# Kernel tuning notes

Hardware: AMD Instinct MI355X
Metric: run time of the kernel (lower is better)

Reference implementation:

```python
import jax, jax.numpy as jnp
import numpy as np

NUM_CEPS = 13  # default num_ceps in log_mel_to_cepstral


def _dct_basis(n_mels, num_ceps):
    # Orthonormal DCT-II basis (scipy.fftpack.dct type=2, norm='ortho'),
    # truncated to the first num_ceps rows. Shape (num_ceps, n_mels).
    n = jnp.arange(n_mels, dtype=jnp.float32)
    k = jnp.arange(num_ceps, dtype=jnp.float32)
    basis = jnp.cos(jnp.pi * (n[None, :] + 0.5) * k[:, None] / n_mels)
    scale = jnp.where(k == 0, jnp.sqrt(1.0 / n_mels), jnp.sqrt(2.0 / n_mels))
    return basis * scale[:, None]


def _log_mel_to_cepstral(mel, basis):
    # mel: (B, 1, F, T) -> cepstral (B, num_ceps, T) with CMVN over (B*T)
    x = jnp.log1p(jnp.abs(mel[:, 0]))                 # (B, F, T)
    c = jnp.einsum('kf,bft->bkt', basis, x)           # (B, num_ceps, T)
    mean = jnp.mean(c, axis=(0, 2), keepdims=True)
    # torch .std is unbiased (ddof=1) over the B*T flattened samples
    std = jnp.std(c, axis=(0, 2), keepdims=True, ddof=1) + 1e-6
    return (c - mean) / std


def setup_inputs() -> dict:
    key = jax.random.key(0)
    k1, k2 = jax.random.split(key)
    B, F, T = 64, 128, 4096
    mel_true = jax.random.normal(k1, (B, 1, F, T), dtype=jnp.float32)
    mel_pred = jax.random.normal(k2, (B, 1, F, T), dtype=jnp.float32)
    return {"mel_true": mel_true, "mel_pred": mel_pred}


def reference(mel_true, mel_pred):
    n_mels = mel_true.shape[2]
    basis = _dct_basis(n_mels, NUM_CEPS)
    c_true = _log_mel_to_cepstral(mel_true, basis)
    c_pred = _log_mel_to_cepstral(mel_pred, basis)
    diff = c_true - c_pred
    mse_dist = jnp.sum(diff * diff, axis=1)           # (B, T)
    log_base_10 = 10.0 / jnp.log(jnp.float32(10.0))
    mcd = log_base_10 * jnp.sqrt(2.0 * mse_dist)
    return jnp.mean(mcd)
```

## Files before the change

### kernel.cpp

```cpp
#include <hip/hip_runtime.h>
#include <math.h>

#define BB 64
#define FF 128
#define TT 4096
#define KK 13
#define NT (BB * TT)
#define NPAIR (NT / 2)
#define MCD_C  6.14185100f



#define KLIST(X) X(0) X(1) X(2) X(3) X(4) X(5) X(6) X(7) X(8) X(9) X(10) X(11) X(12)
#define K12(X)        X(1) X(2) X(3) X(4) X(5) X(6) X(7) X(8) X(9) X(10) X(11) X(12)

__global__ __launch_bounds__(256)
__attribute__((amdgpu_waves_per_eu(4, 4)))
void pass1_kernel(
    const float* __restrict__ melT, const float* __restrict__ melP,
    float* __restrict__ sums, float* __restrict__ cT, float* __restrict__ cP)
{
    const int tensor = blockIdx.x >> 9;
    const int gp = ((blockIdx.x & 511) << 8) + threadIdx.x;
    const float* __restrict__ src = tensor ? melP : melT;
    float* __restrict__ dst = tensor ? cP : cT;

    const int g0 = gp << 1;
    const int b  = g0 >> 12;
    const int t0 = g0 & (TT - 1);
    const float* p = src + (size_t)b * (FF * TT) + t0;

#define DECLACC(i) float ax##i = 0.f, ay##i = 0.f;
    KLIST(DECLACC)
#undef DECLACC

    for (int f0 = 0; f0 < FF; f0 += 8) {
        float2 v[8];
#pragma unroll
        for (int j = 0; j < 8; ++j)
            v[j] = *(const float2*)(p + (size_t)(f0 + j) * TT);

#pragma unroll
        for (int j = 0; j < 8; ++j) {
            const float xx = __log2f(1.0f + fabsf(v[j].x));
            const float xy = __log2f(1.0f + fabsf(v[j].y));

            const float b1 = __cosf((3.14159265358979f / 128.0f) *
                                    ((float)(f0 + j) + 0.5f));
            const float tw = b1 + b1;
            const float b2  = fmaf(tw, b1,  -1.0f);
            const float b3  = fmaf(tw, b2,  -b1);
            const float b4  = fmaf(tw, b3,  -b2);
            const float b5  = fmaf(tw, b4,  -b3);
            const float b6  = fmaf(tw, b5,  -b4);
            const float b7  = fmaf(tw, b6,  -b5);
            const float b8  = fmaf(tw, b7,  -b6);
            const float b9  = fmaf(tw, b8,  -b7);
            const float b10 = fmaf(tw, b9,  -b8);
            const float b11 = fmaf(tw, b10, -b9);
            const float b12 = fmaf(tw, b11, -b10);

            ax0 += xx; ay0 += xy;
#define FMAK(i) ax##i = fmaf(b##i, xx, ax##i); ay##i = fmaf(b##i, xy, ay##i);
            K12(FMAK)
#undef FMAK
        }
    }

#define STK(i) ((float2*)(dst + (size_t)(i) * NT))[gp] = make_float2(ax##i, ay##i);
    KLIST(STK)
#undef STK

    __shared__ float red[4][26];
    const int lane = threadIdx.x & 63;
    const int wave = threadIdx.x >> 6;
#define REDK(i) { \
        float s = ax##i + ay##i; \
        float q = fmaf(ax##i, ax##i, ay##i * ay##i); \
        for (int o = 32; o > 0; o >>= 1) { \
            s += __shfl_down(s, o); q += __shfl_down(q, o); } \
        if (lane == 0) { red[wave][i] = s; red[wave][13 + i] = q; } }
    KLIST(REDK)
#undef REDK
    __syncthreads();
    if (threadIdx.x < 26) {
        const float v = red[0][threadIdx.x] + red[1][threadIdx.x] +
                        red[2][threadIdx.x] + red[3][threadIdx.x];
        atomicAdd(&sums[(tensor * 26 + threadIdx.x) * 16], v);
    }
}

__global__ __launch_bounds__(256, 4) void pass2_kernel(
    const float* __restrict__ sums, const float* __restrict__ cT,
    const float* __restrict__ cP, float* __restrict__ partials)
{
    __shared__ float mT[13], iT[13], mP[13], iP[13];
    if (threadIdx.x < 26) {
        const int tns = threadIdx.x >= 13;
        const int k   = threadIdx.x - tns * 13;
        const float s = sums[(tns * 26 + k) * 16];
        const float q = sums[(tns * 26 + 13 + k) * 16];
        const float N = (float)NT;
        const float m = s / N;
        const float var = fmaxf((q - s * m) / (N - 1.0f), 0.0f);
        const float isd = 1.0f / (sqrtf(var) + 1e-6f);
        if (tns == 0) { mT[k] = m; iT[k] = isd; }
        else          { mP[k] = m; iP[k] = isd; }
    }
    __syncthreads();

    const int gp = blockIdx.x * 256 + threadIdx.x;
    float ssx = 0.0f, ssy = 0.0f;
#pragma unroll
    for (int k = 0; k < KK; ++k) {
        const float2 a = ((const float2*)(cT + (size_t)k * NT))[gp];
        const float2 p = ((const float2*)(cP + (size_t)k * NT))[gp];
        const float dx = (a.x - mT[k]) * iT[k] - (p.x - mP[k]) * iP[k];
        const float dy = (a.y - mT[k]) * iT[k] - (p.y - mP[k]) * iP[k];
        ssx = fmaf(dx, dx, ssx);
        ssy = fmaf(dy, dy, ssy);
    }
    float v = MCD_C * (sqrtf(ssx) + sqrtf(ssy));

    const int lane = threadIdx.x & 63;
    const int wave = threadIdx.x >> 6;
    for (int o = 32; o > 0; o >>= 1) v += __shfl_down(v, o);
    __shared__ float r2[4];
    if (lane == 0) r2[wave] = v;
    __syncthreads();
    if (threadIdx.x == 0)
        partials[blockIdx.x] = r2[0] + r2[1] + r2[2] + r2[3];
}

__global__ __launch_bounds__(256) void pass3_kernel(
    const float* __restrict__ partials, float* __restrict__ out)
{
    float v = partials[threadIdx.x] + partials[threadIdx.x + 256];
    const int lane = threadIdx.x & 63;
    const int wave = threadIdx.x >> 6;
    for (int o = 32; o > 0; o >>= 1) v += __shfl_down(v, o);
    __shared__ float r2[4];
    if (lane == 0) r2[wave] = v;
    __syncthreads();
    if (threadIdx.x == 0)
        out[0] = (r2[0] + r2[1] + r2[2] + r2[3]) * (1.0f / (float)NT);
}

extern "C" void kernel_launch(void* const* d_in, const int* in_sizes, int n_in,
                              void* d_out, int out_size, void* d_ws, size_t ws_size,
                              hipStream_t stream) {
    const float* melT = (const float*)d_in[0];
    const float* melP = (const float*)d_in[1];
    float* out      = (float*)d_out;
    float* sums     = (float*)d_ws;
    float* partials = (float*)((char*)d_ws + 4096);
    float* cT       = (float*)((char*)d_ws + 8192);
    float* cP       = cT + (size_t)KK * NT;

    hipMemsetAsync(d_ws, 0, 4096, stream);

    pass1_kernel<<<1024, 256, 0, stream>>>(melT, melP, sums, cT, cP);
    pass2_kernel<<<512, 256, 0, stream>>>(sums, cT, cP, partials);
    pass3_kernel<<<1, 256, 0, stream>>>(partials, out);
}
```

Before: 287.3 us.

## Fuse MCD passes into one cooperative kernel with grid sync, keeping cepstra in registers

Replaces the three-pass pipeline with a single cooperative kernel. Each thread handles one time column for both tensors, keeps its 13 cepstral coefficients in registers, and after a grid-wide sync applies CMVN and the MCD reduction. This removes the intermediate cepstral writes and re-reads (about 27 MB of traffic) and two kernel launches. The costs are a grid barrier, double the per-thread register state, and a fallback path that recomputes everything if the cooperative launch fails. Reductions now use DPP instead of shuffles.

```diff
diff --git a/kernel.cpp b/kernel.cpp
--- a/kernel.cpp
+++ b/kernel.cpp
@@ -1,149 +1,200 @@
 #include <hip/hip_runtime.h>
+#include <hip/hip_cooperative_groups.h>
 #include <math.h>
+
+namespace cg = cooperative_groups;
 
 #define BB 64
 #define FF 128
 #define TT 4096
 #define KK 13
 #define NT (BB * TT)
-#define NPAIR (NT / 2)
+#define NBLK 1024
 #define MCD_C  6.14185100f
 
 
-
-#define KLIST(X) X(0) X(1) X(2) X(3) X(4) X(5) X(6) X(7) X(8) X(9) X(10) X(11) X(12)
-#define K12(X)        X(1) X(2) X(3) X(4) X(5) X(6) X(7) X(8) X(9) X(10) X(11) X(12)
-
-__global__ __launch_bounds__(256)
-__attribute__((amdgpu_waves_per_eu(4, 4)))
-void pass1_kernel(
-    const float* __restrict__ melT, const float* __restrict__ melP,
-    float* __restrict__ sums, float* __restrict__ cT, float* __restrict__ cP)
-{
-    const int tensor = blockIdx.x >> 9;
-    const int gp = ((blockIdx.x & 511) << 8) + threadIdx.x;
-    const float* __restrict__ src = tensor ? melP : melT;
-    float* __restrict__ dst = tensor ? cP : cT;
-
-    const int g0 = gp << 1;
-    const int b  = g0 >> 12;
-    const int t0 = g0 & (TT - 1);
-    const float* p = src + (size_t)b * (FF * TT) + t0;
-
-#define DECLACC(i) float ax##i = 0.f, ay##i = 0.f;
-    KLIST(DECLACC)
-#undef DECLACC
-
-    for (int f0 = 0; f0 < FF; f0 += 8) {
-        float2 v[8];
-#pragma unroll
-        for (int j = 0; j < 8; ++j)
-            v[j] = *(const float2*)(p + (size_t)(f0 + j) * TT);
-
-#pragma unroll
-        for (int j = 0; j < 8; ++j) {
-            const float xx = __log2f(1.0f + fabsf(v[j].x));
-            const float xy = __log2f(1.0f + fabsf(v[j].y));
-
-            const float b1 = __cosf((3.14159265358979f / 128.0f) *
-                                    ((float)(f0 + j) + 0.5f));
-            const float tw = b1 + b1;
-            const float b2  = fmaf(tw, b1,  -1.0f);
-            const float b3  = fmaf(tw, b2,  -b1);
-            const float b4  = fmaf(tw, b3,  -b2);
-            const float b5  = fmaf(tw, b4,  -b3);
-            const float b6  = fmaf(tw, b5,  -b4);
-            const float b7  = fmaf(tw, b6,  -b5);
-            const float b8  = fmaf(tw, b7,  -b6);
-            const float b9  = fmaf(tw, b8,  -b7);
-            const float b10 = fmaf(tw, b9,  -b8);
-            const float b11 = fmaf(tw, b10, -b9);
-            const float b12 = fmaf(tw, b11, -b10);
-
-            ax0 += xx; ay0 += xy;
-#define FMAK(i) ax##i = fmaf(b##i, xx, ax##i); ay##i = fmaf(b##i, xy, ay##i);
-            K12(FMAK)
-#undef FMAK
+template <int CTRL>
+__device__ __forceinline__ float dpp_add(float x) {
+    return x + __int_as_float(__builtin_amdgcn_update_dpp(
+                   0, __float_as_int(x), CTRL, 0xf, 0xf, true));
+}
+__device__ __forceinline__ float wave_sum(float x) {
+    x = dpp_add<0x111>(x);
+    x = dpp_add<0x112>(x);
+    x = dpp_add<0x114>(x);
+    x = dpp_add<0x118>(x);
+    x = dpp_add<0x142>(x);
+    x = dpp_add<0x143>(x);
+    return x;
+}
+
+__device__ __forceinline__ float agent_load(const float* p) {
+    return __hip_atomic_load(p, __ATOMIC_RELAXED, __HIP_MEMORY_SCOPE_AGENT);
+}
+
+__device__ __forceinline__ void load8(const float* __restrict__ p, int f0,
+                                      float (&v)[8]) {
+#pragma unroll
+    for (int j = 0; j < 8; ++j) v[j] = p[(size_t)(f0 + j) * TT];
+}
+
+__device__ __forceinline__ void comp8(int f0, const float (&vT)[8],
+                                      const float (&vP)[8],
+                                      float (&aT)[KK], float (&aP)[KK]) {
+#pragma unroll
+    for (int j = 0; j < 8; ++j) {
+        const float xT = __log2f(1.0f + fabsf(vT[j]));
+        const float xP = __log2f(1.0f + fabsf(vP[j]));
+        float bk[KK];
+        bk[0] = 1.0f;
+        bk[1] = __cosf((3.14159265358979f / 128.0f) * ((float)(f0 + j) + 0.5f));
+        const float tw = bk[1] + bk[1];
+#pragma unroll
+        for (int k = 2; k < KK; ++k) bk[k] = fmaf(tw, bk[k - 1], -bk[k - 2]);
+#pragma unroll
+        for (int k = 0; k < KK; ++k) {
+            aT[k] = fmaf(bk[k], xT, aT[k]);
+            aP[k] = fmaf(bk[k], xP, aP[k]);
         }
     }
-
-#define STK(i) ((float2*)(dst + (size_t)(i) * NT))[gp] = make_float2(ax##i, ay##i);
-    KLIST(STK)
-#undef STK
-
-    __shared__ float red[4][26];
-    const int lane = threadIdx.x & 63;
-    const int wave = threadIdx.x >> 6;
-#define REDK(i) { \
-        float s = ax##i + ay##i; \
-        float q = fmaf(ax##i, ax##i, ay##i * ay##i); \
-        for (int o = 32; o > 0; o >>= 1) { \
-            s += __shfl_down(s, o); q += __shfl_down(q, o); } \
-        if (lane == 0) { red[wave][i] = s; red[wave][13 + i] = q; } }
-    KLIST(REDK)
-#undef REDK
+}
+
+__device__ __forceinline__ void accum_col(const float* __restrict__ pT,
+                                          const float* __restrict__ pP,
+                                          float (&aT)[KK], float (&aP)[KK]) {
+#pragma unroll
+    for (int k = 0; k < KK; ++k) { aT[k] = 0.0f; aP[k] = 0.0f; }
+    float vT0[8], vP0[8], vT1[8], vP1[8];
+    load8(pT, 0, vT0); load8(pP, 0, vP0);
+#pragma unroll 1
+    for (int f0 = 0; f0 < FF - 16; f0 += 16) {
+        load8(pT, f0 + 8, vT1);  load8(pP, f0 + 8, vP1);
+        comp8(f0, vT0, vP0, aT, aP);
+        load8(pT, f0 + 16, vT0); load8(pP, f0 + 16, vP0);
+        comp8(f0 + 8, vT1, vP1, aT, aP);
+    }
+    load8(pT, FF - 8, vT1); load8(pP, FF - 8, vP1);
+    comp8(FF - 16, vT0, vP0, aT, aP);
+    comp8(FF - 8, vT1, vP1, aT, aP);
+}
+
+__device__ __forceinline__ void block_stats(const float (&aT)[KK],
+                                            const float (&aP)[KK],
+                                            int tid, float* __restrict__ sums) {
+    const int lane = tid & 63;
+    const int wave = tid >> 6;
+    __shared__ float red[4][52];
+#pragma unroll
+    for (int k = 0; k < KK; ++k) {
+        const float s0 = wave_sum(aT[k]);
+        const float s1 = wave_sum(aT[k] * aT[k]);
+        const float s2 = wave_sum(aP[k]);
+        const float s3 = wave_sum(aP[k] * aP[k]);
+        if (lane == 63) {
+            red[wave][k]      = s0; red[wave][13 + k] = s1;
+            red[wave][26 + k] = s2; red[wave][39 + k] = s3;
+        }
+    }
     __syncthreads();
-    if (threadIdx.x < 26) {
-        const float v = red[0][threadIdx.x] + red[1][threadIdx.x] +
-                        red[2][threadIdx.x] + red[3][threadIdx.x];
-        atomicAdd(&sums[(tensor * 26 + threadIdx.x) * 16], v);
-    }
-}
-
-__global__ __launch_bounds__(256, 4) void pass2_kernel(
-    const float* __restrict__ sums, const float* __restrict__ cT,
-    const float* __restrict__ cP, float* __restrict__ partials)
-{
-    __shared__ float mT[13], iT[13], mP[13], iP[13];
-    if (threadIdx.x < 26) {
-        const int tns = threadIdx.x >= 13;
-        const int k   = threadIdx.x - tns * 13;
-        const float s = sums[(tns * 26 + k) * 16];
-        const float q = sums[(tns * 26 + 13 + k) * 16];
+    if (tid < 52) {
+        const float v = red[0][tid] + red[1][tid] + red[2][tid] + red[3][tid];
+        atomicAdd(&sums[tid * 16], v);
+    }
+}
+
+__device__ __forceinline__ void finalize_stats(int tid,
+                                               const float* __restrict__ sums,
+                                               float (&mS)[2][KK],
+                                               float (&iS)[2][KK]) {
+    if (tid < 26) {
+        const int tns = tid >= 13;
+        const int k   = tid - tns * 13;
+        const float s = agent_load(&sums[(tns * 26 + k) * 16]);
+        const float q = agent_load(&sums[(tns * 26 + 13 + k) * 16]);
         const float N = (float)NT;
         const float m = s / N;
         const float var = fmaxf((q - s * m) / (N - 1.0f), 0.0f);
-        const float isd = 1.0f / (sqrtf(var) + 1e-6f);
-        if (tns == 0) { mT[k] = m; iT[k] = isd; }
-        else          { mP[k] = m; iP[k] = isd; }
+        mS[tns][k] = m;
+        iS[tns][k] = 1.0f / (sqrtf(var) + 1e-6f);
     }
     __syncthreads();
-
-    const int gp = blockIdx.x * 256 + threadIdx.x;
-    float ssx = 0.0f, ssy = 0.0f;
+}
+
+__device__ __forceinline__ void mcd_epilogue(const float (&aT)[KK],
+                                             const float (&aP)[KK],
+                                             int tid, const float (&mS)[2][KK],
+                                             const float (&iS)[2][KK],
+                                             float* __restrict__ out) {
+    float ss = 0.0f;
 #pragma unroll
     for (int k = 0; k < KK; ++k) {
-        const float2 a = ((const float2*)(cT + (size_t)k * NT))[gp];
-        const float2 p = ((const float2*)(cP + (size_t)k * NT))[gp];
-        const float dx = (a.x - mT[k]) * iT[k] - (p.x - mP[k]) * iP[k];
-        const float dy = (a.y - mT[k]) * iT[k] - (p.y - mP[k]) * iP[k];
-        ssx = fmaf(dx, dx, ssx);
-        ssy = fmaf(dy, dy, ssy);
-    }
-    float v = MCD_C * (sqrtf(ssx) + sqrtf(ssy));
-
-    const int lane = threadIdx.x & 63;
-    const int wave = threadIdx.x >> 6;
-    for (int o = 32; o > 0; o >>= 1) v += __shfl_down(v, o);
+        const float d = (aT[k] - mS[0][k]) * iS[0][k]
+                      - (aP[k] - mS[1][k]) * iS[1][k];
+        ss = fmaf(d, d, ss);
+    }
+    float v = wave_sum(MCD_C * sqrtf(ss));
+    const int lane = tid & 63;
+    const int wave = tid >> 6;
     __shared__ float r2[4];
-    if (lane == 0) r2[wave] = v;
+    if (lane == 63) r2[wave] = v;
     __syncthreads();
-    if (threadIdx.x == 0)
-        partials[blockIdx.x] = r2[0] + r2[1] + r2[2] + r2[3];
-}
-
-__global__ __launch_bounds__(256) void pass3_kernel(
-    const float* __restrict__ partials, float* __restrict__ out)
+    if (tid == 0)
+        atomicAdd(out, (r2[0] + r2[1] + r2[2] + r2[3]) * (1.0f / (float)NT));
+}
+
+__global__ __launch_bounds__(256)
+__attribute__((amdgpu_waves_per_eu(4)))
+void mcd_fused(const float* __restrict__ melT, const float* __restrict__ melP,
+               float* __restrict__ sums, float* __restrict__ out)
 {
-    float v = partials[threadIdx.x] + partials[threadIdx.x + 256];
-    const int lane = threadIdx.x & 63;
-    const int wave = threadIdx.x >> 6;
-    for (int o = 32; o > 0; o >>= 1) v += __shfl_down(v, o);
-    __shared__ float r2[4];
-    if (lane == 0) r2[wave] = v;
-    __syncthreads();
-    if (threadIdx.x == 0)
-        out[0] = (r2[0] + r2[1] + r2[2] + r2[3]) * (1.0f / (float)NT);
+    const int tid = threadIdx.x;
+    const int col = blockIdx.x * 256 + tid;
+    const int b   = col >> 12;
+    const int t   = col & (TT - 1);
+    const size_t base = (size_t)b * (size_t)(FF * TT) + (size_t)t;
+
+    float aT[KK], aP[KK];
+    accum_col(melT + base, melP + base, aT, aP);
+    block_stats(aT, aP, tid, sums);
+
+    __threadfence();
+    cg::this_grid().sync();
+
+    __shared__ float mS[2][KK], iS[2][KK];
+    finalize_stats(tid, sums, mS, iS);
+    mcd_epilogue(aT, aP, tid, mS, iS, out);
+}
+
+__global__ __launch_bounds__(256)
+__attribute__((amdgpu_waves_per_eu(4)))
+void stats_kernel(const float* __restrict__ melT, const float* __restrict__ melP,
+                  float* __restrict__ sums)
+{
+    const int tid = threadIdx.x;
+    const int col = blockIdx.x * 256 + tid;
+    const int b   = col >> 12;
+    const int t   = col & (TT - 1);
+    const size_t base = (size_t)b * (size_t)(FF * TT) + (size_t)t;
+    float aT[KK], aP[KK];
+    accum_col(melT + base, melP + base, aT, aP);
+    block_stats(aT, aP, tid, sums);
+}
+
+__global__ __launch_bounds__(256)
+__attribute__((amdgpu_waves_per_eu(4)))
+void final_kernel(const float* __restrict__ melT, const float* __restrict__ melP,
+                  const float* __restrict__ sums, float* __restrict__ out)
+{
+    const int tid = threadIdx.x;
+    const int col = blockIdx.x * 256 + tid;
+    const int b   = col >> 12;
+    const int t   = col & (TT - 1);
+    const size_t base = (size_t)b * (size_t)(FF * TT) + (size_t)t;
+    float aT[KK], aP[KK];
+    accum_col(melT + base, melP + base, aT, aP);
+    __shared__ float mS[2][KK], iS[2][KK];
+    finalize_stats(tid, sums, mS, iS);
+    mcd_epilogue(aT, aP, tid, mS, iS, out);
 }
 
 extern "C" void kernel_launch(void* const* d_in, const int* in_sizes, int n_in,
@@ -151,15 +202,18 @@
                               hipStream_t stream) {
     const float* melT = (const float*)d_in[0];
     const float* melP = (const float*)d_in[1];
-    float* out      = (float*)d_out;
-    float* sums     = (float*)d_ws;
-    float* partials = (float*)((char*)d_ws + 4096);
-    float* cT       = (float*)((char*)d_ws + 8192);
-    float* cP       = cT + (size_t)KK * NT;
+    float* sums = (float*)d_ws;
+    float* out  = (float*)d_out;
 
     hipMemsetAsync(d_ws, 0, 4096, stream);
-
-    pass1_kernel<<<1024, 256, 0, stream>>>(melT, melP, sums, cT, cP);
-    pass2_kernel<<<512, 256, 0, stream>>>(sums, cT, cP, partials);
-    pass3_kernel<<<1, 256, 0, stream>>>(partials, out);
-}
+    hipMemsetAsync(d_out, 0, sizeof(float), stream);
+
+    void* args[] = { (void*)&melT, (void*)&melP, (void*)&sums, (void*)&out };
+    hipError_t err = hipLaunchCooperativeKernel(
+        (const void*)mcd_fused, dim3(NBLK), dim3(256), args, 0, stream);
+    if (err != hipSuccess) {
+        (void)hipGetLastError();
+        stats_kernel<<<NBLK, 256, 0, stream>>>(melT, melP, sums);
+        final_kernel<<<NBLK, 256, 0, stream>>>(melT, melP, sums, out);
+    }
+}
```

Measured after the change: 555.6 us. 1.93x slower.

## Split mel-bin loop across half-waves, use DPP reductions, drop final reduce kernel

Applied to the files above, without the earlier changes.

The first pass now assigns each time-pair to two half-waves that each cover 64 of the 128 mel bins, then merge their accumulators with a cross-half shuffle. This doubles the grid and raises the occupancy target to expose more parallelism for the log/DCT work. Wave reductions now use DPP row operations, with a 0.5 scale to cancel the duplicated halves. The second pass switches to scalar per-column loads and atomically adds into the output, so the third reduction kernel goes away. The cost is an extra memset, redundant work in the merged halves, and float atomics that give a non-deterministic summation order.

```diff
diff --git a/kernel.cpp b/kernel.cpp
--- a/kernel.cpp
+++ b/kernel.cpp
@@ -10,31 +10,50 @@
 #define MCD_C  6.14185100f
 
 
-
 #define KLIST(X) X(0) X(1) X(2) X(3) X(4) X(5) X(6) X(7) X(8) X(9) X(10) X(11) X(12)
 #define K12(X)        X(1) X(2) X(3) X(4) X(5) X(6) X(7) X(8) X(9) X(10) X(11) X(12)
 
+template <int CTRL>
+__device__ __forceinline__ float dpp_add(float x) {
+    return x + __int_as_float(__builtin_amdgcn_update_dpp(
+                   0, __float_as_int(x), CTRL, 0xf, 0xf, true));
+}
+__device__ __forceinline__ float wave_sum(float x) {
+    x = dpp_add<0x111>(x);
+    x = dpp_add<0x112>(x);
+    x = dpp_add<0x114>(x);
+    x = dpp_add<0x118>(x);
+    x = dpp_add<0x142>(x);
+    x = dpp_add<0x143>(x);
+    return x;
+}
+
 __global__ __launch_bounds__(256)
-__attribute__((amdgpu_waves_per_eu(4, 4)))
+__attribute__((amdgpu_waves_per_eu(8, 8)))
 void pass1_kernel(
     const float* __restrict__ melT, const float* __restrict__ melP,
     float* __restrict__ sums, float* __restrict__ cT, float* __restrict__ cP)
 {
-    const int tensor = blockIdx.x >> 9;
-    const int gp = ((blockIdx.x & 511) << 8) + threadIdx.x;
+    const int tensor = blockIdx.x >> 10;
+    const int tid  = threadIdx.x;
+    const int lane = tid & 63;
+    const int wave = tid >> 6;
+    const int half = lane >> 5;
+    const int gp = (blockIdx.x & 1023) * 128 + wave * 32 + (lane & 31);
     const float* __restrict__ src = tensor ? melP : melT;
     float* __restrict__ dst = tensor ? cP : cT;
 
     const int g0 = gp << 1;
     const int b  = g0 >> 12;
     const int t0 = g0 & (TT - 1);
-    const float* p = src + (size_t)b * (FF * TT) + t0;
+    const int fbase = half << 6;
+    const float* p = src + (size_t)b * (FF * TT) + (size_t)fbase * TT + t0;
 
 #define DECLACC(i) float ax##i = 0.f, ay##i = 0.f;
     KLIST(DECLACC)
 #undef DECLACC
 
-    for (int f0 = 0; f0 < FF; f0 += 8) {
+    for (int f0 = 0; f0 < 64; f0 += 8) {
         float2 v[8];
 #pragma unroll
         for (int j = 0; j < 8; ++j)
@@ -46,7 +65,7 @@
             const float xy = __log2f(1.0f + fabsf(v[j].y));
 
             const float b1 = __cosf((3.14159265358979f / 128.0f) *
-                                    ((float)(f0 + j) + 0.5f));
+                                    ((float)(fbase + f0 + j) + 0.5f));
             const float tw = b1 + b1;
             const float b2  = fmaf(tw, b1,  -1.0f);
             const float b3  = fmaf(tw, b2,  -b1);
@@ -67,34 +86,35 @@
         }
     }
 
+#define MRG(i) ax##i += __shfl_xor(ax##i, 32); ay##i += __shfl_xor(ay##i, 32);
+    KLIST(MRG)
+#undef MRG
+
+    if (half == 0) {
 #define STK(i) ((float2*)(dst + (size_t)(i) * NT))[gp] = make_float2(ax##i, ay##i);
-    KLIST(STK)
+        KLIST(STK)
 #undef STK
+    }
 
     __shared__ float red[4][26];
-    const int lane = threadIdx.x & 63;
-    const int wave = threadIdx.x >> 6;
 #define REDK(i) { \
-        float s = ax##i + ay##i; \
-        float q = fmaf(ax##i, ax##i, ay##i * ay##i); \
-        for (int o = 32; o > 0; o >>= 1) { \
-            s += __shfl_down(s, o); q += __shfl_down(q, o); } \
-        if (lane == 0) { red[wave][i] = s; red[wave][13 + i] = q; } }
+        float s = wave_sum(ax##i + ay##i); \
+        float q = wave_sum(fmaf(ax##i, ax##i, ay##i * ay##i)); \
+        if (lane == 63) { red[wave][i] = s; red[wave][13 + i] = q; } }
     KLIST(REDK)
 #undef REDK
     __syncthreads();
-    if (threadIdx.x < 26) {
-        const float v = red[0][threadIdx.x] + red[1][threadIdx.x] +
-                        red[2][threadIdx.x] + red[3][threadIdx.x];
-        atomicAdd(&sums[(tensor * 26 + threadIdx.x) * 16], v);
+    if (tid < 26) {
+        const float v = red[0][tid] + red[1][tid] + red[2][tid] + red[3][tid];
+        atomicAdd(&sums[(tensor * 26 + tid) * 16], 0.5f * v);
     }
 }
 
-__global__ __launch_bounds__(256, 4) void pass2_kernel(
+__global__ __launch_bounds__(256) void pass2_kernel(
     const float* __restrict__ sums, const float* __restrict__ cT,
-    const float* __restrict__ cP, float* __restrict__ partials)
+    const float* __restrict__ cP, float* __restrict__ out)
 {
-    __shared__ float mT[13], iT[13], mP[13], iP[13];
+    __shared__ float mS[2][13], iS[2][13];
     if (threadIdx.x < 26) {
         const int tns = threadIdx.x >= 13;
         const int k   = threadIdx.x - tns * 13;
@@ -103,47 +123,29 @@
         const float N = (float)NT;
         const float m = s / N;
         const float var = fmaxf((q - s * m) / (N - 1.0f), 0.0f);
-        const float isd = 1.0f / (sqrtf(var) + 1e-6f);
-        if (tns == 0) { mT[k] = m; iT[k] = isd; }
-        else          { mP[k] = m; iP[k] = isd; }
+        mS[tns][k] = m;
+        iS[tns][k] = 1.0f / (sqrtf(var) + 1e-6f);
     }
     __syncthreads();
 
-    const int gp = blockIdx.x * 256 + threadIdx.x;
-    float ssx = 0.0f, ssy = 0.0f;
+    const int col = blockIdx.x * 256 + threadIdx.x;
+    float ss = 0.0f;
 #pragma unroll
     for (int k = 0; k < KK; ++k) {
-        const float2 a = ((const float2*)(cT + (size_t)k * NT))[gp];
-        const float2 p = ((const float2*)(cP + (size_t)k * NT))[gp];
-        const float dx = (a.x - mT[k]) * iT[k] - (p.x - mP[k]) * iP[k];
-        const float dy = (a.y - mT[k]) * iT[k] - (p.y - mP[k]) * iP[k];
-        ssx = fmaf(dx, dx, ssx);
-        ssy = fmaf(dy, dy, ssy);
+        const float a = cT[(size_t)k * NT + col];
+        const float p = cP[(size_t)k * NT + col];
+        const float d = (a - mS[0][k]) * iS[0][k] - (p - mS[1][k]) * iS[1][k];
+        ss = fmaf(d, d, ss);
     }
-    float v = MCD_C * (sqrtf(ssx) + sqrtf(ssy));
+    float v = wave_sum(MCD_C * sqrtf(ss));
 
     const int lane = threadIdx.x & 63;
     const int wave = threadIdx.x >> 6;
-    for (int o = 32; o > 0; o >>= 1) v += __shfl_down(v, o);
     __shared__ float r2[4];
-    if (lane == 0) r2[wave] = v;
+    if (lane == 63) r2[wave] = v;
     __syncthreads();
     if (threadIdx.x == 0)
-        partials[blockIdx.x] = r2[0] + r2[1] + r2[2] + r2[3];
-}
-
-__global__ __launch_bounds__(256) void pass3_kernel(
-    const float* __restrict__ partials, float* __restrict__ out)
-{
-    float v = partials[threadIdx.x] + partials[threadIdx.x + 256];
-    const int lane = threadIdx.x & 63;
-    const int wave = threadIdx.x >> 6;
-    for (int o = 32; o > 0; o >>= 1) v += __shfl_down(v, o);
-    __shared__ float r2[4];
-    if (lane == 0) r2[wave] = v;
-    __syncthreads();
-    if (threadIdx.x == 0)
-        out[0] = (r2[0] + r2[1] + r2[2] + r2[3]) * (1.0f / (float)NT);
+        atomicAdd(out, (r2[0] + r2[1] + r2[2] + r2[3]) * (1.0f / (float)NT));
 }
 
 extern "C" void kernel_launch(void* const* d_in, const int* in_sizes, int n_in,
@@ -151,15 +153,14 @@
                               hipStream_t stream) {
     const float* melT = (const float*)d_in[0];
     const float* melP = (const float*)d_in[1];
-    float* out      = (float*)d_out;
-    float* sums     = (float*)d_ws;
-    float* partials = (float*)((char*)d_ws + 4096);
-    float* cT       = (float*)((char*)d_ws + 8192);
-    float* cP       = cT + (size_t)KK * NT;
+    float* out  = (float*)d_out;
+    float* sums = (float*)d_ws;
+    float* cT   = (float*)((char*)d_ws + 8192);
+    float* cP   = cT + (size_t)KK * NT;
 
     hipMemsetAsync(d_ws, 0, 4096, stream);
+    hipMemsetAsync(d_out, 0, sizeof(float), stream);
 
-    pass1_kernel<<<1024, 256, 0, stream>>>(melT, melP, sums, cT, cP);
-    pass2_kernel<<<512, 256, 0, stream>>>(sums, cT, cP, partials);
-    pass3_kernel<<<1, 256, 0, stream>>>(partials, out);
+    pass1_kernel<<<2048, 256, 0, stream>>>(melT, melP, sums, cT, cP);
+    pass2_kernel<<<1024, 256, 0, stream>>>(sums, cT, cP, out);
 }
```

Result: slower. 309.4 us (+7.7%).
